# Kernel optimization log

Measured on AMD Instinct MI355X. Metric: run time of the kernel, lower is better.

## Reference

```python
import jax, jax.numpy as jnp
import numpy as np

B, T, DM, DS = 8, 2048, 1024, 256
BASE_DECAY = 0.05


def _lin(k, out_dim, in_dim):
    return jax.random.normal(k, (out_dim, in_dim), jnp.float32) / np.sqrt(in_dim).astype(np.float32)


def setup_inputs() -> dict:
    key = jax.random.key(0)
    ks = jax.random.split(key, 18)
    return {
        "x": jax.random.normal(ks[0], (B, T, DM), jnp.float32),
        "prev_state": jax.random.normal(ks[1], (B, DS), jnp.float32),
        "W_in": _lin(ks[2], DS, DM),
        "W_x": _lin(ks[3], DS, DM),
        "W_s": _lin(ks[4], DS, DS),
        "W_out": _lin(ks[5], DM, DS),
        "W_gx": _lin(ks[6], DS, DM),
        "b_gx": jax.random.normal(ks[7], (DS,), jnp.float32) * 0.02,
        "W_gs": _lin(ks[8], DS, DS),
        "b_gs": jax.random.normal(ks[9], (DS,), jnp.float32) * 0.02,
        "W_dc": _lin(ks[10], DS, DM + DS),
        "b_dc": jax.random.normal(ks[11], (DS,), jnp.float32) * 0.02,
        "W_pp": _lin(ks[12], DS, 2 * DS),
        "b_pp": jax.random.normal(ks[13], (DS,), jnp.float32) * 0.02,
        "W_pg": _lin(ks[14], DS, DS),
        "b_pg": jax.random.normal(ks[15], (DS,), jnp.float32) * 0.02,
    }


def reference(x, prev_state, W_in, W_x, W_s, W_out, W_gx, b_gx, W_gs, b_gs,
              W_dc, b_dc, W_pp, b_pp, W_pg, b_pg):
    # torch Linear: y = x @ W.T (+ b); W is [out, in]
    lin = lambda v, W: jnp.einsum('bti,oi->bto', v, W)
    Bx, Tx, _ = x.shape
    delta = lin(x, W_in)                                   # [B,T,DS]
    s_prev = jnp.broadcast_to(prev_state[:, None, :], (Bx, Tx, prev_state.shape[-1]))
    ctx = jnp.concatenate([x, s_prev], axis=-1)            # [B,T,DM+DS]
    decay = jnp.exp(-BASE_DECAY * jnp.clip(jax.nn.sigmoid(lin(ctx, W_dc) + b_dc), 0.0, 1.0))
    s_pred = s_prev * decay + delta + lin(x, W_x) + 0.5 * lin(s_prev, W_s)
    perturb_in = jnp.concatenate([s_pred, s_prev], axis=-1)  # [B,T,2*DS]
    perturb_vec = jnp.tanh(lin(perturb_in, W_pp) + b_pp)
    perturb_strength = jax.nn.sigmoid(lin(s_prev, W_pg) + b_pg)
    s_corrected = s_pred + perturb_strength * perturb_vec
    gate_in = jax.nn.sigmoid(lin(x, W_gx) + b_gx)
    gate_state = jax.nn.sigmoid(lin(s_prev, W_gs) + b_gs)
    h = s_corrected * gate_in * gate_state
    out = lin(h, W_out)                                    # [B,T,DM]
    return out, h[:, -1, :]
```

## Files before the change

### kernel.cpp

```cpp
#include <hip/hip_runtime.h>
#include <hip/hip_bf16.h>
#include <math.h>


typedef __attribute__((ext_vector_type(4)))  float f32x4;
typedef __attribute__((ext_vector_type(8)))  short bf16x8;

#define DEV static __device__ __forceinline__

DEV float bf2f(short u) {
  union { float f; unsigned i; } v; v.i = ((unsigned)(unsigned short)u) << 16; return v.f;
}
DEV short f2bf(float f) {
  union { float f; unsigned i; } v; v.f = f;
  unsigned x = v.i;
  return (short)((x + 0x7fffu + ((x >> 16) & 1u)) >> 16);
}
DEV unsigned pk_bf16(float lo, float hi) {
  __hip_bfloat162 h = __float22bfloat162_rn(make_float2(lo, hi));
  return *(unsigned*)&h;
}
DEV float sigmoidf_(float x) { return 1.f / (1.f + expf(-x)); }

DEV void gl16(const void* g, void* l) {
  __builtin_amdgcn_global_load_lds(
      (const __attribute__((address_space(1))) void*)(g),
      (__attribute__((address_space(3))) void*)(l), 16, 0, 0);
}

static const size_t OFF_S    = 0;
static const size_t OFF_G    = 8388608;
static const size_t OFF_XBF  = 25165824;
static const size_t OFF_WCAT = OFF_XBF + 33554432;
static const size_t OFF_WPP  = OFF_WCAT + 1572864;
static const size_t OFF_WOUT = OFF_WPP + 131072;
static const size_t OFF_VEC  = OFF_WOUT + 524288;

__global__ __launch_bounds__(256, 1) void prep_all_k(
    const float* __restrict__ x, short* __restrict__ xbf,
    const float* __restrict__ W_in, const float* __restrict__ W_x,
    const float* __restrict__ W_gx, const float* __restrict__ W_dc,
    const float* __restrict__ W_pp, const float* __restrict__ W_out,
    short* __restrict__ wcat, short* __restrict__ wpp, short* __restrict__ wout,
    const float* __restrict__ prev, const float* __restrict__ Ws,
    const float* __restrict__ bdc, const float* __restrict__ bpp,
    const float* __restrict__ Wpg, const float* __restrict__ bpg,
    const float* __restrict__ Wgs, const float* __restrict__ bgs,
    float* __restrict__ vecs) {
  const int bid = (int)blockIdx.x, tid = (int)threadIdx.x;
  if (bid < 8192) {
    const size_t i = ((size_t)bid * 256 + tid) * 8;
    const float4 a = *(const float4*)(x + i);
    const float4 b = *(const float4*)(x + i + 4);
    uint4 o;
    o.x = pk_bf16(a.x, a.y); o.y = pk_bf16(a.z, a.w);
    o.z = pk_bf16(b.x, b.y); o.w = pk_bf16(b.z, b.w);
    *(uint4*)(xbf + i) = o;
  } else if (bid < 12544) {
    const int idx = (bid - 8192) * 256 + tid;
    const int N_WCAT = 768 * 1024, N_WPP = 256 * 256;
    if (idx < N_WCAT) {
      const int r = idx >> 10, k = idx & 1023;
      const int g = r / 96, j = r % 96;
      float v;
      if (j < 32)      v = W_in[(g * 32 + j) * 1024 + k] + W_x[(g * 32 + j) * 1024 + k];
      else if (j < 64) v = W_gx[(g * 32 + j - 32) * 1024 + k];
      else             v = W_dc[(g * 32 + j - 64) * 1280 + k];
      wcat[idx] = f2bf(v);
    } else if (idx < N_WCAT + N_WPP) {
      const int j = idx - N_WCAT, o = j >> 8, k = j & 255;
      wpp[j] = f2bf(W_pp[o * 512 + k]);
    } else {
      const int j = idx - N_WCAT - N_WPP, o = j >> 8, k = j & 255;
      wout[j] = f2bf(W_out[o * 256 + k]);
    }
  } else {
    const int sb = bid - 12544;
    const int b = sb / 20, rem = sb % 20, m = rem >> 2, oq = rem & 3;
    const int lane = tid & 63, w = tid >> 6;
    const float4 sv = *(const float4*)(prev + b * 256 + lane * 4);
    const float* Wb; const float* bias; int stride, off;
    if (m == 0)      { Wb = W_dc; stride = 1280; off = 1024; bias = bdc; }
    else if (m == 1) { Wb = Ws;   stride = 256;  off = 0;    bias = nullptr; }
    else if (m == 2) { Wb = W_pp; stride = 512;  off = 256;  bias = bpp; }
    else if (m == 3) { Wb = Wpg;  stride = 256;  off = 0;    bias = bpg; }
    else             { Wb = Wgs;  stride = 256;  off = 0;    bias = bgs; }
    const int o0 = oq * 64 + w * 16;
#pragma unroll 4
    for (int i = 0; i < 16; ++i) {
      const int o = o0 + i;
      const float4 wv = *(const float4*)(Wb + (size_t)o * stride + off + lane * 4);
      float p = wv.x * sv.x + wv.y * sv.y + wv.z * sv.z + wv.w * sv.w;
#pragma unroll
      for (int d = 32; d >= 1; d >>= 1) p += __shfl_xor(p, d, 64);
      if (lane == 0) {
        float r = (m == 1) ? 0.5f * p : p + bias[o];
        if (m >= 3) r = sigmoidf_(r);
        vecs[m * 2048 + b * 256 + o] = r;
      }
    }
  }
}

__global__ __launch_bounds__(256) void gemm1sg_k(const short* __restrict__ A,
                                                 const short* __restrict__ Bm,
                                                 const float* __restrict__ prev,
                                                 const float* __restrict__ bgx,
                                                 const float* __restrict__ vecs,
                                                 short* __restrict__ S,
                                                 short* __restrict__ G) {
  __shared__ short As[2][4096];
  __shared__ short Bs[2][3072];
  const int tid = (int)threadIdx.x, lane = tid & 63, w = tid >> 6;
  int bid = (int)blockIdx.x;
  bid = (bid & 7) * 128 + (bid >> 3);
  const int mt = bid >> 3, ntg = bid & 7;
  const int m0 = mt * 128, b = m0 >> 11;
  const short* gA = A + (size_t)m0 * 1024;
  const short* gB = Bm + (size_t)(ntg * 96) * 1024;
  const int rsub = lane >> 2, kc = (lane & 3) * 8;

  f32x4 acc[2][6];
#pragma unroll
  for (int mi = 0; mi < 2; ++mi)
#pragma unroll
    for (int ni = 0; ni < 6; ++ni)
#pragma unroll
      for (int r = 0; r < 4; ++r) acc[mi][ni][r] = 0.f;

#define STAGE1(buf, t)                                                        \
  {                                                                           \
    _Pragma("unroll")                                                         \
    for (int j = 0; j < 2; ++j) {                                             \
      const int seg = w * 2 + j;                                              \
      gl16(gA + (size_t)(seg * 16 + rsub) * 1024 + (t) * 32 + kc,             \
           As[buf] + seg * 512);                                              \
    }                                                                         \
    {                                                                         \
      const int Gr = w * 64 + lane;                                           \
      gl16(gB + (size_t)(Gr >> 2) * 1024 + (t) * 32 + ((Gr & 3) * 8),         \
           Bs[buf] + w * 512);                                                \
    }                                                                         \
    if (w < 2) {                                                              \
      const int Gr = 256 + w * 64 + lane;                                     \
      gl16(gB + (size_t)(Gr >> 2) * 1024 + (t) * 32 + ((Gr & 3) * 8),         \
           Bs[buf] + 2048 + w * 512);                                         \
    }                                                                         \
  }

  STAGE1(0, 0);
  __syncthreads();
  const int arow = lane & 15, ag = lane >> 4;
#pragma unroll 1
  for (int t = 0; t < 32; ++t) {
    if (t < 31) STAGE1((t + 1) & 1, t + 1);
    const short* Asb = As[t & 1];
    const short* Bsb = Bs[t & 1];
    bf16x8 af[2];
#pragma unroll
    for (int mi = 0; mi < 2; ++mi)
      af[mi] = *(const bf16x8*)(Asb + (w * 32 + mi * 16 + arow) * 32 + ag * 8);
#pragma unroll
    for (int ni = 0; ni < 6; ++ni) {
      const bf16x8 bf = *(const bf16x8*)(Bsb + (ni * 16 + arow) * 32 + ag * 8);
#pragma unroll
      for (int mi = 0; mi < 2; ++mi)
        acc[mi][ni] = __builtin_amdgcn_mfma_f32_16x16x32_bf16(af[mi], bf, acc[mi][ni], 0, 0, 0);
    }
    __syncthreads();
  }
#undef STAGE1

  const int quad = lane >> 4;
#pragma unroll
  for (int nj = 0; nj < 2; ++nj) {
    const int cg = ntg * 32 + nj * 16 + arow;
    const float sdc = vecs[0 * 2048 + b * 256 + cg];
    const float sws = vecs[1 * 2048 + b * 256 + cg];
    const float pv  = prev[b * 256 + cg];
    const float bg  = bgx[cg];
#pragma unroll
    for (int mi = 0; mi < 2; ++mi)
#pragma unroll
      for (int r = 0; r < 4; ++r) {
        const int row = m0 + w * 32 + mi * 16 + quad * 4 + r;
        const float dec = expf(-0.05f * sigmoidf_(acc[mi][4 + nj][r] + sdc));
        const float sp = pv * dec + acc[mi][nj][r] + sws;
        const float g = sigmoidf_(acc[mi][2 + nj][r] + bg);
        S[(size_t)row * 256 + cg] = f2bf(sp);
        G[(size_t)row * 256 + cg] = f2bf(g);
      }
  }
}

__global__ __launch_bounds__(256) void gemm2h_k(const short* __restrict__ S,
                                                const short* __restrict__ G,
                                                const short* __restrict__ Wpp,
                                                const float* __restrict__ vecs,
                                                short* __restrict__ H,
                                                float* __restrict__ out) {
  __shared__ short As[2][2048];
  __shared__ short Bs[2][4096];
  const int tid = (int)threadIdx.x, lane = tid & 63, w = tid >> 6;
  const int wr = w >> 1, wc = w & 1;
  int bid = (int)blockIdx.x;
  bid = (bid & 7) * 64 + (bid >> 3);
  const int m0 = (bid >> 1) * 64, n0 = (bid & 1) * 128;
  const int b = m0 >> 11;
  const short* gA = S + (size_t)m0 * 256;
  const short* gB = Wpp + (size_t)n0 * 256;

  f32x4 acc[2][4];
#pragma unroll
  for (int mi = 0; mi < 2; ++mi)
#pragma unroll
    for (int ni = 0; ni < 4; ++ni)
#pragma unroll
      for (int r = 0; r < 4; ++r) acc[mi][ni][r] = 0.f;

#define STAGE2(buf, t)                                                        \
  {                                                                           \
    {                                                                         \
      const int g = tid;                                                      \
      gl16(gA + (size_t)(g >> 2) * 256 + (t) * 32 + (g & 3) * 8,              \
           As[buf] + w * 512);                                                \
    }                                                                         \
    _Pragma("unroll")                                                         \
    for (int j = 0; j < 2; ++j) {                                             \
      const int g = j * 256 + tid;                                            \
      gl16(gB + (size_t)(g >> 2) * 256 + (t) * 32 + (g & 3) * 8,              \
           Bs[buf] + (j * 256 + w * 64) * 8);                                 \
    }                                                                         \
  }

  STAGE2(0, 0);
  __syncthreads();
  const int arow = lane & 15, ag = lane >> 4;
#pragma unroll 1
  for (int t = 0; t < 8; ++t) {
    if (t < 7) STAGE2((t + 1) & 1, t + 1);
    const short* Asb = As[t & 1];
    const short* Bsb = Bs[t & 1];
    bf16x8 af[2], bfv[4];
#pragma unroll
    for (int mi = 0; mi < 2; ++mi)
      af[mi] = *(const bf16x8*)(Asb + (wr * 32 + mi * 16 + arow) * 32 + ag * 8);
#pragma unroll
    for (int ni = 0; ni < 4; ++ni)
      bfv[ni] = *(const bf16x8*)(Bsb + (wc * 64 + ni * 16 + arow) * 32 + ag * 8);
#pragma unroll
    for (int mi = 0; mi < 2; ++mi)
#pragma unroll
      for (int ni = 0; ni < 4; ++ni)
        acc[mi][ni] = __builtin_amdgcn_mfma_f32_16x16x32_bf16(af[mi], bfv[ni], acc[mi][ni], 0, 0, 0);
    __syncthreads();
  }
#undef STAGE2

#pragma unroll
  for (int mi = 0; mi < 2; ++mi)
#pragma unroll
    for (int ni = 0; ni < 4; ++ni) {
      const int col = n0 + wc * 64 + ni * 16 + (lane & 15);
      const float spp  = vecs[2 * 2048 + b * 256 + col];
      const float pstr = vecs[3 * 2048 + b * 256 + col];
      const float gst  = vecs[4 * 2048 + b * 256 + col];
#pragma unroll
      for (int r = 0; r < 4; ++r) {
        const int row = m0 + wr * 32 + mi * 16 + (lane >> 4) * 4 + r;
        const float pv = tanhf(acc[mi][ni][r] + spp);
        const float sp = bf2f(S[(size_t)row * 256 + col]);
        const float h = (sp + pstr * pv) * bf2f(G[(size_t)row * 256 + col]) * gst;
        H[(size_t)row * 256 + col] = f2bf(h);
        if ((row & 2047) == 2047) out[16777216 + b * 256 + col] = h;
      }
    }
}

__global__ __launch_bounds__(256) void gemm3_k(const short* __restrict__ H,
                                               const short* __restrict__ Wout,
                                               float* __restrict__ out) {
  __shared__ short As[2][2048];
  __shared__ short Bs[2][8192];
  const int tid = (int)threadIdx.x, lane = tid & 63, w = tid >> 6;
  const int wr = w >> 1, wc = w & 1;
  int bid = (int)blockIdx.x;
  bid = (bid & 7) * 128 + (bid >> 3);
  const int m0 = (bid >> 2) * 64, n0 = (bid & 3) * 256;
  const short* gA = H + (size_t)m0 * 256;
  const short* gB = Wout + (size_t)n0 * 256;

  f32x4 acc[2][8];
#pragma unroll
  for (int mi = 0; mi < 2; ++mi)
#pragma unroll
    for (int ni = 0; ni < 8; ++ni)
#pragma unroll
      for (int r = 0; r < 4; ++r) acc[mi][ni][r] = 0.f;

#define STAGE3(buf, t)                                                        \
  {                                                                           \
    {                                                                         \
      const int g = tid;                                                      \
      gl16(gA + (size_t)(g >> 2) * 256 + (t) * 32 + (g & 3) * 8,              \
           As[buf] + w * 512);                                                \
    }                                                                         \
    _Pragma("unroll")                                                         \
    for (int j = 0; j < 4; ++j) {                                             \
      const int g = j * 256 + tid;                                            \
      gl16(gB + (size_t)(g >> 2) * 256 + (t) * 32 + (g & 3) * 8,              \
           Bs[buf] + (j * 256 + w * 64) * 8);                                 \
    }                                                                         \
  }

  STAGE3(0, 0);
  __syncthreads();
  const int arow = lane & 15, ag = lane >> 4;
#pragma unroll 1
  for (int t = 0; t < 8; ++t) {
    if (t < 7) STAGE3((t + 1) & 1, t + 1);
    const short* Asb = As[t & 1];
    const short* Bsb = Bs[t & 1];
    bf16x8 af[2], bfv[8];
#pragma unroll
    for (int mi = 0; mi < 2; ++mi)
      af[mi] = *(const bf16x8*)(Asb + (wr * 32 + mi * 16 + arow) * 32 + ag * 8);
#pragma unroll
    for (int ni = 0; ni < 8; ++ni)
      bfv[ni] = *(const bf16x8*)(Bsb + (wc * 128 + ni * 16 + arow) * 32 + ag * 8);
#pragma unroll
    for (int mi = 0; mi < 2; ++mi)
#pragma unroll
      for (int ni = 0; ni < 8; ++ni)
        acc[mi][ni] = __builtin_amdgcn_mfma_f32_16x16x32_bf16(af[mi], bfv[ni], acc[mi][ni], 0, 0, 0);
    __syncthreads();
  }
#undef STAGE3

#pragma unroll
  for (int mi = 0; mi < 2; ++mi)
#pragma unroll
    for (int ni = 0; ni < 8; ++ni) {
      const int col = n0 + wc * 128 + ni * 16 + (lane & 15);
#pragma unroll
      for (int r = 0; r < 4; ++r) {
        const int row = m0 + wr * 32 + mi * 16 + (lane >> 4) * 4 + r;
        out[(size_t)row * 1024 + col] = acc[mi][ni][r];
      }
    }
}

extern "C" void kernel_launch(void* const* d_in, const int* in_sizes, int n_in,
                              void* d_out, int out_size, void* d_ws, size_t ws_size,
                              hipStream_t stream) {
  (void)in_sizes; (void)n_in; (void)out_size; (void)ws_size;
  const float* x      = (const float*)d_in[0];
  const float* prev   = (const float*)d_in[1];
  const float* W_in   = (const float*)d_in[2];
  const float* W_x    = (const float*)d_in[3];
  const float* W_s    = (const float*)d_in[4];
  const float* W_out  = (const float*)d_in[5];
  const float* W_gx   = (const float*)d_in[6];
  const float* b_gx   = (const float*)d_in[7];
  const float* W_gs   = (const float*)d_in[8];
  const float* b_gs   = (const float*)d_in[9];
  const float* W_dc   = (const float*)d_in[10];
  const float* b_dc   = (const float*)d_in[11];
  const float* W_pp   = (const float*)d_in[12];
  const float* b_pp   = (const float*)d_in[13];
  const float* W_pg   = (const float*)d_in[14];
  const float* b_pg   = (const float*)d_in[15];

  char* ws = (char*)d_ws;
  short* S    = (short*)(ws + OFF_S);
  short* G    = (short*)(ws + OFF_G);
  short* xbf  = (short*)(ws + OFF_XBF);
  short* H    = (short*)(ws + OFF_XBF);
  short* wcat = (short*)(ws + OFF_WCAT);
  short* wpp  = (short*)(ws + OFF_WPP);
  short* wout = (short*)(ws + OFF_WOUT);
  float* vecs = (float*)(ws + OFF_VEC);
  float* out  = (float*)d_out;

  prep_all_k<<<12704, 256, 0, stream>>>(x, xbf, W_in, W_x, W_gx, W_dc, W_pp, W_out,
                                        wcat, wpp, wout, prev, W_s, b_dc, b_pp,
                                        W_pg, b_pg, W_gs, b_gs, vecs);
  gemm1sg_k<<<1024, 256, 0, stream>>>(xbf, wcat, prev, b_gx, vecs, S, G);
  gemm2h_k<<<512, 256, 0, stream>>>(S, G, wpp, vecs, H, out);
  gemm3_k<<<1024, 256, 0, stream>>>(H, wout, out);
}
```

Baseline: 104.8 us.

## Replace first GEMM with 256x256 eight-wave pipelined kernel and separate elementwise epilogue

The fused GEMM1 with 128x96 tiles and a gating epilogue is replaced by a large-tile 256x256 GEMM. It uses 512 threads, a four-buffer LDS pipeline, XOR-swizzled LDS addressing, explicit waitcnt and barrier scheduling, and raised wave priority around the MFMAs. The weight concatenation is reordered into contiguous blocks. The decay, gate and state math moves into a new elementwise kernel that reads a bf16 intermediate Y. This aims to cut redundant global and LDS traffic per FLOP, at the cost of an extra 25MB intermediate round trip, another launch, and only 192 blocks, each using 128KB of LDS.

```diff
diff --git a/kernel.cpp b/kernel.cpp
--- a/kernel.cpp
+++ b/kernel.cpp
@@ -28,9 +28,10 @@
       (__attribute__((address_space(3))) void*)(l), 16, 0, 0);
 }
 
-static const size_t OFF_S    = 0;
-static const size_t OFF_G    = 8388608;
+static const size_t OFF_Y    = 0;
 static const size_t OFF_XBF  = 25165824;
+static const size_t OFF_S    = OFF_XBF;
+static const size_t OFF_G    = OFF_XBF + 8388608;
 static const size_t OFF_WCAT = OFF_XBF + 33554432;
 static const size_t OFF_WPP  = OFF_WCAT + 1572864;
 static const size_t OFF_WOUT = OFF_WPP + 131072;
@@ -61,11 +62,10 @@
     const int N_WCAT = 768 * 1024, N_WPP = 256 * 256;
     if (idx < N_WCAT) {
       const int r = idx >> 10, k = idx & 1023;
-      const int g = r / 96, j = r % 96;
       float v;
-      if (j < 32)      v = W_in[(g * 32 + j) * 1024 + k] + W_x[(g * 32 + j) * 1024 + k];
-      else if (j < 64) v = W_gx[(g * 32 + j - 32) * 1024 + k];
-      else             v = W_dc[(g * 32 + j - 64) * 1280 + k];
+      if (r < 256)      v = W_in[r * 1024 + k] + W_x[r * 1024 + k];
+      else if (r < 512) v = W_gx[(r - 256) * 1024 + k];
+      else              v = W_dc[(r - 512) * 1280 + k];
       wcat[idx] = f2bf(v);
     } else if (idx < N_WCAT + N_WPP) {
       const int j = idx - N_WCAT, o = j >> 8, k = j & 255;
@@ -102,95 +102,137 @@
   }
 }
 
-__global__ __launch_bounds__(256) void gemm1sg_k(const short* __restrict__ A,
-                                                 const short* __restrict__ Bm,
-                                                 const float* __restrict__ prev,
-                                                 const float* __restrict__ bgx,
-                                                 const float* __restrict__ vecs,
-                                                 short* __restrict__ S,
-                                                 short* __restrict__ G) {
-  __shared__ short As[2][4096];
-  __shared__ short Bs[2][3072];
+__global__ __launch_bounds__(512, 2) void gemm1_8p_k(const short* __restrict__ A,
+                                                     const short* __restrict__ Bm,
+                                                     short* __restrict__ Y) {
+  __shared__ short As[4][8192];
+  __shared__ short Bs[4][8192];
   const int tid = (int)threadIdx.x, lane = tid & 63, w = tid >> 6;
+  const int wm = w >> 2, wn = w & 3;
   int bid = (int)blockIdx.x;
-  bid = (bid & 7) * 128 + (bid >> 3);
-  const int mt = bid >> 3, ntg = bid & 7;
-  const int m0 = mt * 128, b = m0 >> 11;
+  bid = (bid & 7) * 24 + (bid >> 3);
+  const int mt = bid / 3, nt = bid % 3;
+  const int m0 = mt * 256;
   const short* gA = A + (size_t)m0 * 1024;
-  const short* gB = Bm + (size_t)(ntg * 96) * 1024;
-  const int rsub = lane >> 2, kc = (lane & 3) * 8;
-
-  f32x4 acc[2][6];
-#pragma unroll
-  for (int mi = 0; mi < 2; ++mi)
-#pragma unroll
-    for (int ni = 0; ni < 6; ++ni)
+  const short* gB = Bm + (size_t)(nt * 256) * 1024;
+
+  f32x4 acc[8][4];
+#pragma unroll
+  for (int mi = 0; mi < 8; ++mi)
+#pragma unroll
+    for (int ni = 0; ni < 4; ++ni)
 #pragma unroll
       for (int r = 0; r < 4; ++r) acc[mi][ni][r] = 0.f;
 
-#define STAGE1(buf, t)                                                        \
+#define STG(gax, lds, half, t)                                                \
   {                                                                           \
     _Pragma("unroll")                                                         \
     for (int j = 0; j < 2; ++j) {                                             \
-      const int seg = w * 2 + j;                                              \
-      gl16(gA + (size_t)(seg * 16 + rsub) * 1024 + (t) * 32 + kc,             \
-           As[buf] + seg * 512);                                              \
+      const int G = j * 512 + tid, r = G >> 3, g = G & 7;                     \
+      gl16(gax + (size_t)((half) * 128 + r) * 1024 + (t) * 64 +               \
+               ((g ^ (r & 7)) * 8),                                           \
+           (lds) + G * 8);                                                    \
     }                                                                         \
-    {                                                                         \
-      const int Gr = w * 64 + lane;                                           \
-      gl16(gB + (size_t)(Gr >> 2) * 1024 + (t) * 32 + ((Gr & 3) * 8),         \
-           Bs[buf] + w * 512);                                                \
-    }                                                                         \
-    if (w < 2) {                                                              \
-      const int Gr = 256 + w * 64 + lane;                                     \
-      gl16(gB + (size_t)(Gr >> 2) * 1024 + (t) * 32 + ((Gr & 3) * 8),         \
-           Bs[buf] + 2048 + w * 512);                                         \
-    }                                                                         \
-  }
-
-  STAGE1(0, 0);
-  __syncthreads();
+  }
+
+  STG(gA, As[0], 0, 0); STG(gA, As[1], 1, 0);
+  STG(gB, Bs[0], 0, 0); STG(gB, Bs[1], 1, 0);
+  STG(gA, As[2], 0, 1);
+  asm volatile("s_waitcnt vmcnt(2)" ::: "memory");
+  __builtin_amdgcn_s_barrier();
+
   const int arow = lane & 15, ag = lane >> 4;
+  bf16x8 af[4][2], bfv[2][2];
 #pragma unroll 1
-  for (int t = 0; t < 32; ++t) {
-    if (t < 31) STAGE1((t + 1) & 1, t + 1);
-    const short* Asb = As[t & 1];
-    const short* Bsb = Bs[t & 1];
-    bf16x8 af[2];
-#pragma unroll
-    for (int mi = 0; mi < 2; ++mi)
-      af[mi] = *(const bf16x8*)(Asb + (w * 32 + mi * 16 + arow) * 32 + ag * 8);
-#pragma unroll
-    for (int ni = 0; ni < 6; ++ni) {
-      const bf16x8 bf = *(const bf16x8*)(Bsb + (ni * 16 + arow) * 32 + ag * 8);
-#pragma unroll
-      for (int mi = 0; mi < 2; ++mi)
-        acc[mi][ni] = __builtin_amdgcn_mfma_f32_16x16x32_bf16(af[mi], bf, acc[mi][ni], 0, 0, 0);
-    }
-    __syncthreads();
-  }
-#undef STAGE1
-
-  const int quad = lane >> 4;
-#pragma unroll
-  for (int nj = 0; nj < 2; ++nj) {
-    const int cg = ntg * 32 + nj * 16 + arow;
-    const float sdc = vecs[0 * 2048 + b * 256 + cg];
-    const float sws = vecs[1 * 2048 + b * 256 + cg];
-    const float pv  = prev[b * 256 + cg];
-    const float bg  = bgx[cg];
-#pragma unroll
-    for (int mi = 0; mi < 2; ++mi)
+  for (int t = 0; t < 16; ++t) {
+    const short* sA = As[(2 * t + wm) & 3];
+    const short* sB = Bs[(2 * t + (wn >> 1)) & 3];
+#pragma unroll
+    for (int q = 0; q < 4; ++q) {
+      const int qm = q >> 1, qn = q & 1;
+      if (qn == 0) {
+#pragma unroll
+        for (int fi = 0; fi < 4; ++fi) {
+          const int r = qm * 64 + fi * 16 + arow;
+#pragma unroll
+          for (int ks = 0; ks < 2; ++ks)
+            af[fi][ks] = *(const bf16x8*)(sA + r * 64 + (((ks * 4 + ag) ^ (r & 7)) << 3));
+        }
+      }
+#pragma unroll
+      for (int fj = 0; fj < 2; ++fj) {
+        const int r = (wn & 1) * 64 + qn * 32 + fj * 16 + arow;
+#pragma unroll
+        for (int ks = 0; ks < 2; ++ks)
+          bfv[fj][ks] = *(const bf16x8*)(sB + r * 64 + (((ks * 4 + ag) ^ (r & 7)) << 3));
+      }
+      if (q == 0) {
+        if (t + 1 < 16) {
+          STG(gB, Bs[(2 * t + 2) & 3], 0, t + 1);
+          STG(gA, As[(2 * t + 3) & 3], 1, t + 1);
+          STG(gB, Bs[(2 * t + 3) & 3], 1, t + 1);
+        }
+      } else if (q == 3) {
+        if (t + 2 < 16) STG(gA, As[(2 * t + 4) & 3], 0, t + 2);
+        if (t <= 13)      { asm volatile("s_waitcnt vmcnt(2)" ::: "memory"); }
+        else if (t == 14) { asm volatile("s_waitcnt vmcnt(0)" ::: "memory"); }
+      }
+      __builtin_amdgcn_s_barrier();
+      asm volatile("s_waitcnt lgkmcnt(0)" ::: "memory");
+      __builtin_amdgcn_sched_barrier(0);
+      __builtin_amdgcn_s_setprio(1);
+#pragma unroll
+      for (int fi = 0; fi < 4; ++fi)
+#pragma unroll
+        for (int fj = 0; fj < 2; ++fj)
+#pragma unroll
+          for (int ks = 0; ks < 2; ++ks)
+            acc[qm * 4 + fi][qn * 2 + fj] = __builtin_amdgcn_mfma_f32_16x16x32_bf16(
+                af[fi][ks], bfv[fj][ks], acc[qm * 4 + fi][qn * 2 + fj], 0, 0, 0);
+      __builtin_amdgcn_s_setprio(0);
+      __builtin_amdgcn_s_barrier();
+    }
+  }
+#undef STG
+
+#pragma unroll
+  for (int mi = 0; mi < 8; ++mi)
+#pragma unroll
+    for (int ni = 0; ni < 4; ++ni) {
+      const int col = nt * 256 + wn * 64 + ni * 16 + (lane & 15);
 #pragma unroll
       for (int r = 0; r < 4; ++r) {
-        const int row = m0 + w * 32 + mi * 16 + quad * 4 + r;
-        const float dec = expf(-0.05f * sigmoidf_(acc[mi][4 + nj][r] + sdc));
-        const float sp = pv * dec + acc[mi][nj][r] + sws;
-        const float g = sigmoidf_(acc[mi][2 + nj][r] + bg);
-        S[(size_t)row * 256 + cg] = f2bf(sp);
-        G[(size_t)row * 256 + cg] = f2bf(g);
-      }
-  }
+        const int row = m0 + wm * 128 + mi * 16 + (lane >> 4) * 4 + r;
+        Y[(size_t)row * 768 + col] = f2bf(acc[mi][ni][r]);
+      }
+    }
+}
+
+__global__ __launch_bounds__(256, 1) void elem1_k(const short* __restrict__ Y,
+                                                  const float* __restrict__ prev,
+                                                  const float* __restrict__ bgx,
+                                                  const float* __restrict__ vecs,
+                                                  short* __restrict__ S,
+                                                  short* __restrict__ G) {
+  const int t = (int)blockIdx.x * 256 + (int)threadIdx.x;
+  const int row = t >> 5, gi = t & 31, j0 = gi * 8;
+  const int b = row >> 11;
+  const short* yr = Y + (size_t)row * 768;
+  const bf16x8 yix = *(const bf16x8*)(yr + j0);
+  const bf16x8 ygx = *(const bf16x8*)(yr + 256 + j0);
+  const bf16x8 ydc = *(const bf16x8*)(yr + 512 + j0);
+  bf16x8 so, go;
+#pragma unroll
+  for (int j = 0; j < 8; ++j) {
+    const int c = b * 256 + j0 + j;
+    const float dcl = bf2f(ydc[j]) + vecs[0 * 2048 + c];
+    const float dec = expf(-0.05f * sigmoidf_(dcl));
+    const float sp = prev[c] * dec + bf2f(yix[j]) + vecs[1 * 2048 + c];
+    const float g = sigmoidf_(bf2f(ygx[j]) + bgx[j0 + j]);
+    so[j] = f2bf(sp); go[j] = f2bf(g);
+  }
+  *(bf16x8*)(S + (size_t)row * 256 + j0) = so;
+  *(bf16x8*)(G + (size_t)row * 256 + j0) = go;
 }
 
 __global__ __launch_bounds__(256) void gemm2h_k(const short* __restrict__ S,
@@ -199,8 +241,8 @@
                                                 const float* __restrict__ vecs,
                                                 short* __restrict__ H,
                                                 float* __restrict__ out) {
-  __shared__ short As[2][2048];
-  __shared__ short Bs[2][4096];
+  __shared__ short As2[2][2048];
+  __shared__ short Bs2[2][4096];
   const int tid = (int)threadIdx.x, lane = tid & 63, w = tid >> 6;
   const int wr = w >> 1, wc = w & 1;
   int bid = (int)blockIdx.x;
@@ -223,13 +265,13 @@
     {                                                                         \
       const int g = tid;                                                      \
       gl16(gA + (size_t)(g >> 2) * 256 + (t) * 32 + (g & 3) * 8,              \
-           As[buf] + w * 512);                                                \
+           As2[buf] + w * 512);                                               \
     }                                                                         \
     _Pragma("unroll")                                                         \
     for (int j = 0; j < 2; ++j) {                                             \
       const int g = j * 256 + tid;                                            \
       gl16(gB + (size_t)(g >> 2) * 256 + (t) * 32 + (g & 3) * 8,              \
-           Bs[buf] + (j * 256 + w * 64) * 8);                                 \
+           Bs2[buf] + (j * 256 + w * 64) * 8);                                \
     }                                                                         \
   }
 
@@ -239,8 +281,8 @@
 #pragma unroll 1
   for (int t = 0; t < 8; ++t) {
     if (t < 7) STAGE2((t + 1) & 1, t + 1);
-    const short* Asb = As[t & 1];
-    const short* Bsb = Bs[t & 1];
+    const short* Asb = As2[t & 1];
+    const short* Bsb = Bs2[t & 1];
     bf16x8 af[2], bfv[4];
 #pragma unroll
     for (int mi = 0; mi < 2; ++mi)
@@ -280,8 +322,8 @@
 __global__ __launch_bounds__(256) void gemm3_k(const short* __restrict__ H,
                                                const short* __restrict__ Wout,
                                                float* __restrict__ out) {
-  __shared__ short As[2][2048];
-  __shared__ short Bs[2][8192];
+  __shared__ short As3[2][2048];
+  __shared__ short Bs3[2][8192];
   const int tid = (int)threadIdx.x, lane = tid & 63, w = tid >> 6;
   const int wr = w >> 1, wc = w & 1;
   int bid = (int)blockIdx.x;
@@ -303,13 +345,13 @@
     {                                                                         \
       const int g = tid;                                                      \
       gl16(gA + (size_t)(g >> 2) * 256 + (t) * 32 + (g & 3) * 8,              \
-           As[buf] + w * 512);                                                \
+           As3[buf] + w * 512);                                               \
     }                                                                         \
     _Pragma("unroll")                                                         \
     for (int j = 0; j < 4; ++j) {                                             \
       const int g = j * 256 + tid;                                            \
       gl16(gB + (size_t)(g >> 2) * 256 + (t) * 32 + (g & 3) * 8,              \
-           Bs[buf] + (j * 256 + w * 64) * 8);                                 \
+           Bs3[buf] + (j * 256 + w * 64) * 8);                                \
     }                                                                         \
   }
 
@@ -319,8 +361,8 @@
 #pragma unroll 1
   for (int t = 0; t < 8; ++t) {
     if (t < 7) STAGE3((t + 1) & 1, t + 1);
-    const short* Asb = As[t & 1];
-    const short* Bsb = Bs[t & 1];
+    const short* Asb = As3[t & 1];
+    const short* Bsb = Bs3[t & 1];
     bf16x8 af[2], bfv[8];
 #pragma unroll
     for (int mi = 0; mi < 2; ++mi)
@@ -372,10 +414,11 @@
   const float* b_pg   = (const float*)d_in[15];
 
   char* ws = (char*)d_ws;
+  short* Y    = (short*)(ws + OFF_Y);
+  short* H    = (short*)(ws + OFF_Y);
+  short* xbf  = (short*)(ws + OFF_XBF);
   short* S    = (short*)(ws + OFF_S);
   short* G    = (short*)(ws + OFF_G);
-  short* xbf  = (short*)(ws + OFF_XBF);
-  short* H    = (short*)(ws + OFF_XBF);
   short* wcat = (short*)(ws + OFF_WCAT);
   short* wpp  = (short*)(ws + OFF_WPP);
   short* wout = (short*)(ws + OFF_WOUT);
@@ -385,7 +428,8 @@
   prep_all_k<<<12704, 256, 0, stream>>>(x, xbf, W_in, W_x, W_gx, W_dc, W_pp, W_out,
                                         wcat, wpp, wout, prev, W_s, b_dc, b_pp,
                                         W_pg, b_pg, W_gs, b_gs, vecs);
-  gemm1sg_k<<<1024, 256, 0, stream>>>(xbf, wcat, prev, b_gx, vecs, S, G);
+  gemm1_8p_k<<<192, 512, 0, stream>>>(xbf, wcat, Y);
+  elem1_k<<<2048, 256, 0, stream>>>(Y, prev, b_gx, vecs, S, G);
   gemm2h_k<<<512, 256, 0, stream>>>(S, G, wpp, vecs, H, out);
   gemm3_k<<<1024, 256, 0, stream>>>(H, wout, out);
 }
```

New measurement: 117.9 us. +12.5%, slower.
